# Kernel optimization log

Hardware: AMD Instinct MI355X
Metric: run time of the kernel (lower is better)

Reference implementation:

```python
import jax, jax.numpy as jnp
import numpy as np
from jax.scipy.special import logsumexp

B, S, D, L = 64, 512, 1024, 9


def setup_inputs() -> dict:
    key = jax.random.key(0)
    k1, k2, k3, k4, k5, k6 = jax.random.split(key, 6)
    inputs = jax.random.normal(k1, (B, S, D), dtype=jnp.float32)
    targets = jax.random.randint(k2, (B, S), 0, L)
    sequence_lengths = jax.random.randint(k3, (B,), S // 2, S + 1)
    mask = (jnp.arange(S)[None, :] < sequence_lengths[:, None])
    W = jax.random.normal(k4, (D, L), dtype=jnp.float32) * (1.0 / np.sqrt(D))
    b = jnp.zeros((L,), dtype=jnp.float32)
    transitions = jax.random.normal(k5, (L, L), dtype=jnp.float32) * 0.1
    return {"inputs": inputs, "targets": targets, "sequence_lengths": sequence_lengths,
            "mask": mask, "W": W, "b": b, "transitions": transitions}


def crf_nll(logits, tags, mask, transitions):
    # logits: [B,S,L], tags: [B,S] int, mask: [B,S] bool, transitions: [L,L]
    maskf = mask.astype(logits.dtype)
    # gold-path score (numerator)
    emit = jnp.take_along_axis(logits, tags[..., None], axis=2)[..., 0]  # [B,S]
    trans = transitions[tags[:, :-1], tags[:, 1:]]                        # [B,S-1]
    numerator = (emit * maskf).sum(-1) + (trans * maskf[:, 1:]).sum(-1)   # [B]
    # partition function via forward algorithm (scan over time)
    alpha0 = logits[:, 0]  # [B,L]; position 0 always valid
    emit_t = jnp.swapaxes(logits[:, 1:], 0, 1)   # [S-1,B,L]
    mask_t = jnp.swapaxes(mask[:, 1:], 0, 1)     # [S-1,B]

    def step(alpha, xs):
        e, m = xs
        scores = alpha[:, :, None] + transitions[None, :, :] + e[:, None, :]  # [B,L,L]
        new = logsumexp(scores, axis=1)                                        # [B,L]
        alpha = jnp.where(m[:, None], new, alpha)
        return alpha, None

    alpha, _ = jax.lax.scan(step, alpha0, (emit_t, mask_t))
    denominator = logsumexp(alpha, axis=-1)  # [B]
    return -(numerator - denominator).sum()


def reference(inputs, targets, sequence_lengths, mask, W, b, transitions):
    logits = jnp.einsum('bsd,dl->bsl', inputs, W) + b  # nn.Linear
    values = crf_nll(logits, targets, mask, transitions)
    return (values, logits)
```

## Files before the change

### kernel.cpp

```cpp
#include <hip/hip_runtime.h>
#include <hip/hip_bf16.h>
#include <math.h>

#define BB 64
#define SS 512
#define DD 1024
#define LL 9
#define NCHUNK 32
#define CLEN 16

#define DPP_ADD(v, ctrl)                                                     \
  v += __int_as_float(__builtin_amdgcn_update_dpp(                           \
      0, __float_as_int(v), ctrl, 0xF, 0xF, false))

__global__ __launch_bounds__(256) void gemm_kernel(
    const float* __restrict__ in, const float* __restrict__ W,
    const float* __restrict__ bias, float* __restrict__ out) {
  __shared__ float Wt[LL][DD];
  int tid = threadIdx.x;
  for (int i = tid; i < DD * LL; i += 256) {
    int k = i / LL, l = i % LL;
    Wt[l][k] = W[i];
  }
  __syncthreads();

  int lane = tid & 63;
  int wave = tid >> 6;
  int p = lane & 15;
  int sub = lane >> 4;

  int r0 = blockIdx.x * 64 + wave * 16 + sub;
  const float* x0 = in + (size_t)r0 * DD;

  float acc[4][LL];
#pragma unroll
  for (int q = 0; q < 4; ++q)
#pragma unroll
    for (int l = 0; l < LL; ++l) acc[q][l] = 0.f;

  for (int it = 0; it < 16; ++it) {
    int k0 = it * 64 + p * 4;
    float4 w4[LL];
#pragma unroll
    for (int l = 0; l < LL; ++l)
      w4[l] = *reinterpret_cast<const float4*>(&Wt[l][k0]);
    float4 a[4];
#pragma unroll
    for (int q = 0; q < 4; ++q)
      a[q] = *reinterpret_cast<const float4*>(x0 + (size_t)q * 4 * DD + k0);
#pragma unroll
    for (int q = 0; q < 4; ++q)
#pragma unroll
      for (int l = 0; l < LL; ++l)
        acc[q][l] += a[q].x * w4[l].x + a[q].y * w4[l].y + a[q].z * w4[l].z +
                     a[q].w * w4[l].w;
  }

#pragma unroll
  for (int q = 0; q < 4; ++q)
#pragma unroll
    for (int l = 0; l < LL; ++l) {
      DPP_ADD(acc[q][l], 0x111);
      DPP_ADD(acc[q][l], 0x112);
      DPP_ADD(acc[q][l], 0x114);
      DPP_ADD(acc[q][l], 0x118);
    }
  if (p == 15) {
#pragma unroll
    for (int q = 0; q < 4; ++q)
#pragma unroll
      for (int l = 0; l < LL; ++l)
        out[(size_t)(r0 + q * 4) * LL + l] = acc[q][l] + bias[l];
  }
}

template <int R>
__device__ inline float swz(float x) {
  return __int_as_float(
      __builtin_amdgcn_ds_swizzle(__float_as_int(x), (R << 10) | 0x1F));
}

__global__ __launch_bounds__(64) void crf_chunk_kernel(
    const float* __restrict__ logits, const int* __restrict__ seqlen,
    const float* __restrict__ trans, float* __restrict__ mats,
    float* __restrict__ scales) {
  int lane = threadIdx.x;
  int j = lane & 15;
  int gid = blockIdx.x * 4 + (lane >> 4);
  int b = gid >> 5;
  int k = gid & 31;
  int len = seqlen[b];

  float Mx[81];
#pragma unroll
  for (int i = 0; i < 81; ++i) Mx[i] = __expf(trans[i]);

  float T[LL];
#pragma unroll
  for (int c = 0; c < LL; ++c) T[c] = (j == c) ? 1.f : 0.f;
  float Cl = 0.f;

  const float* lb = logits + (size_t)b * SS * LL;
  int t0 = k * CLEN + 1;
  int tend = (t0 + CLEN < SS) ? (t0 + CLEN) : SS;

  float e[LL];
#pragma unroll
  for (int c = 0; c < LL; ++c) e[c] = lb[t0 * LL + c];

  for (int t = t0; t < tend; ++t) {
    float Ex[LL];
#pragma unroll
    for (int c = 0; c < LL; ++c) Ex[c] = __expf(e[c]);
    if (t + 1 < tend) {
#pragma unroll
      for (int c = 0; c < LL; ++c) e[c] = lb[(t + 1) * LL + c];
    }
    bool active = (t < len);
    float nT[LL];
#pragma unroll
    for (int c = 0; c < LL; ++c) {
      float s = 0.f;
#pragma unroll
      for (int m = 0; m < LL; ++m) s += T[m] * Mx[m * LL + c];
      nT[c] = s * Ex[c];
    }
#pragma unroll
    for (int c = 0; c < LL; ++c) T[c] = active ? nT[c] : T[c];

    if (((t - t0) & 7) == 7) {
      float m = T[0];
#pragma unroll
      for (int c = 1; c < LL; ++c) m = fmaxf(m, T[c]);
      m = fmaxf(m, swz<1>(m));
      m = fmaxf(m, swz<2>(m));
      m = fmaxf(m, swz<4>(m));
      m = fmaxf(m, swz<8>(m));
      float inv = 1.f / m;
#pragma unroll
      for (int c = 0; c < LL; ++c) T[c] *= inv;
      Cl += __logf(m);
    }
  }
  {
    float m = T[0];
#pragma unroll
    for (int c = 1; c < LL; ++c) m = fmaxf(m, T[c]);
    m = fmaxf(m, swz<1>(m));
    m = fmaxf(m, swz<2>(m));
    m = fmaxf(m, swz<4>(m));
    m = fmaxf(m, swz<8>(m));
    float inv = 1.f / m;
#pragma unroll
    for (int c = 0; c < LL; ++c) T[c] *= inv;
    Cl += __logf(m);
  }

  float* Mg = mats + (size_t)gid * 256;
#pragma unroll
  for (int c = 0; c < 16; ++c)
    Mg[c * 16 + (j ^ c)] = (c < LL) ? T[c] : 0.f;
  if (j == 0) scales[gid] = Cl;
}

__global__ __launch_bounds__(64) void crf_combine_kernel(
    const float* __restrict__ logits, const int* __restrict__ targets,
    const int* __restrict__ seqlen, const float* __restrict__ trans,
    const float* __restrict__ mats, const float* __restrict__ scales,
    float* __restrict__ out_val) {
  int lane = threadIdx.x;
  int j = lane & 15;
  int b = blockIdx.x;
  int len = seqlen[b];
  const float* lb = logits + (size_t)b * SS * LL;
  const float* Mb = mats + (size_t)b * NCHUNK * 256;
  const float* Sb = scales + (size_t)b * NCHUNK;

  float alpha = (j < LL) ? __expf(lb[j]) : 0.f;
  float C = 0.f;

  float4 c0 = *reinterpret_cast<const float4*>(Mb + j * 16 + 0);
  float4 c1 = *reinterpret_cast<const float4*>(Mb + j * 16 + 4);
  float4 c2 = *reinterpret_cast<const float4*>(Mb + j * 16 + 8);
  float4 c3 = *reinterpret_cast<const float4*>(Mb + j * 16 + 12);

  for (int k = 0; k < NCHUNK; ++k) {
    float4 n0, n1, n2, n3;
    if (k + 1 < NCHUNK) {
      const float* Mn = Mb + (size_t)(k + 1) * 256 + j * 16;
      n0 = *reinterpret_cast<const float4*>(Mn + 0);
      n1 = *reinterpret_cast<const float4*>(Mn + 4);
      n2 = *reinterpret_cast<const float4*>(Mn + 8);
      n3 = *reinterpret_cast<const float4*>(Mn + 12);
    }
    float v = alpha * c0.x;
    v += swz<1>(alpha) * c0.y;
    v += swz<2>(alpha) * c0.z;
    v += swz<3>(alpha) * c0.w;
    v += swz<4>(alpha) * c1.x;
    v += swz<5>(alpha) * c1.y;
    v += swz<6>(alpha) * c1.z;
    v += swz<7>(alpha) * c1.w;
    v += swz<8>(alpha) * c2.x;
    v += swz<9>(alpha) * c2.y;
    v += swz<10>(alpha) * c2.z;
    v += swz<11>(alpha) * c2.w;
    v += swz<12>(alpha) * c3.x;
    v += swz<13>(alpha) * c3.y;
    v += swz<14>(alpha) * c3.z;
    v += swz<15>(alpha) * c3.w;
    alpha = v;
    C += Sb[k];

    float m = alpha;
    m = fmaxf(m, swz<1>(m));
    m = fmaxf(m, swz<2>(m));
    m = fmaxf(m, swz<4>(m));
    m = fmaxf(m, swz<8>(m));
    float inv = 1.f / m;
    alpha *= inv;
    C += __logf(m);

    if (k + 1 < NCHUNK) { c0 = n0; c1 = n1; c2 = n2; c3 = n3; }
  }

  float s = alpha;
  s += swz<1>(s);
  s += swz<2>(s);
  s += swz<4>(s);
  s += swz<8>(s);
  float denom = C + __logf(s);

  float num = 0.f;
  const int* tb = targets + (size_t)b * SS;
  for (int t = lane; t < SS; t += 64) {
    if (t < len) {
      int tg = tb[t];
      num += lb[t * LL + tg];
      if (t >= 1) {
        int tgp = tb[t - 1];
        num += trans[tgp * LL + tg];
      }
    }
  }
  num += __shfl_xor(num, 1, 64);
  num += __shfl_xor(num, 2, 64);
  num += __shfl_xor(num, 4, 64);
  num += __shfl_xor(num, 8, 64);
  num += __shfl_xor(num, 16, 64);
  num += __shfl_xor(num, 32, 64);

  if (lane == 0) atomicAdd(out_val, denom - num);
}

extern "C" void kernel_launch(void* const* d_in, const int* in_sizes, int n_in,
                              void* d_out, int out_size, void* d_ws,
                              size_t ws_size, hipStream_t stream) {
  const float* inputs = (const float*)d_in[0];
  const int* targets = (const int*)d_in[1];
  const int* seqlen = (const int*)d_in[2];
  const float* W = (const float*)d_in[4];
  const float* bias = (const float*)d_in[5];
  const float* trans = (const float*)d_in[6];
  float* out = (float*)d_out;

  float* mats = (float*)d_ws;
  float* scales = mats + (size_t)BB * NCHUNK * 256;

  gemm_kernel<<<512, 256, 0, stream>>>(inputs, W, bias, out + 1);
  crf_chunk_kernel<<<BB * NCHUNK / 4, 64, 0, stream>>>(out + 1, seqlen, trans,
                                                       mats, scales);
  hipMemsetAsync(d_out, 0, sizeof(float), stream);
  crf_combine_kernel<<<BB, 64, 0, stream>>>(out + 1, targets, seqlen, trans,
                                            mats, scales, out);
}
```

Measured before the change: 56.19 us.

## Prefetch GEMM inputs, move numerator into chunk kernel, drop memset via counter reduction

The GEMM kernel now double-buffers its global input loads, fetching the next iteration's float4s before computing the current one. The gold-path numerator is computed per chunk in the chunk kernel. The combine kernel sums scales and numerator partials with one wave reduction, rescales alpha only every fourth chunk, and uses a tree-shaped sum in its matvec. The memset and float atomicAdd are replaced by per-batch partials plus a last-block counter reduction. This removes a launch and serial work from the combine tail, at the cost of extra registers in the GEMM and reliance on threadfence and counter ordering.

```diff
diff --git a/kernel.cpp b/kernel.cpp
--- a/kernel.cpp
+++ b/kernel.cpp
@@ -19,7 +19,7 @@
   __shared__ float Wt[LL][DD];
   int tid = threadIdx.x;
   for (int i = tid; i < DD * LL; i += 256) {
-    int k = i / LL, l = i % LL;
+    int k = i / LL, l = i - k * LL;
     Wt[l][k] = W[i];
   }
   __syncthreads();
@@ -30,7 +30,7 @@
   int sub = lane >> 4;
 
   int r0 = blockIdx.x * 64 + wave * 16 + sub;
-  const float* x0 = in + (size_t)r0 * DD;
+  const float* x0 = in + (size_t)r0 * DD + p * 4;
 
   float acc[4][LL];
 #pragma unroll
@@ -38,22 +38,33 @@
 #pragma unroll
     for (int l = 0; l < LL; ++l) acc[q][l] = 0.f;
 
+  float4 a[4], an[4];
+#pragma unroll
+  for (int q = 0; q < 4; ++q)
+    a[q] = *reinterpret_cast<const float4*>(x0 + (size_t)q * 4 * DD);
+
   for (int it = 0; it < 16; ++it) {
+    if (it < 15) {
+#pragma unroll
+      for (int q = 0; q < 4; ++q)
+        an[q] = *reinterpret_cast<const float4*>(x0 + (size_t)q * 4 * DD +
+                                                 (it + 1) * 64);
+    }
     int k0 = it * 64 + p * 4;
     float4 w4[LL];
 #pragma unroll
     for (int l = 0; l < LL; ++l)
       w4[l] = *reinterpret_cast<const float4*>(&Wt[l][k0]);
-    float4 a[4];
-#pragma unroll
-    for (int q = 0; q < 4; ++q)
-      a[q] = *reinterpret_cast<const float4*>(x0 + (size_t)q * 4 * DD + k0);
 #pragma unroll
     for (int q = 0; q < 4; ++q)
 #pragma unroll
       for (int l = 0; l < LL; ++l)
         acc[q][l] += a[q].x * w4[l].x + a[q].y * w4[l].y + a[q].z * w4[l].z +
                      a[q].w * w4[l].w;
+    if (it < 15) {
+#pragma unroll
+      for (int q = 0; q < 4; ++q) a[q] = an[q];
+    }
   }
 
 #pragma unroll
@@ -81,9 +92,12 @@
 }
 
 __global__ __launch_bounds__(64) void crf_chunk_kernel(
-    const float* __restrict__ logits, const int* __restrict__ seqlen,
-    const float* __restrict__ trans, float* __restrict__ mats,
-    float* __restrict__ scales) {
+    const float* __restrict__ logits, const int* __restrict__ targets,
+    const int* __restrict__ seqlen, const float* __restrict__ trans,
+    float* __restrict__ mats, float* __restrict__ scales,
+    float* __restrict__ numpart, unsigned* __restrict__ counter) {
+  if (blockIdx.x == 0 && threadIdx.x == 0) *counter = 0u;
+
   int lane = threadIdx.x;
   int j = lane & 15;
   int gid = blockIdx.x * 4 + (lane >> 4);
@@ -101,6 +115,7 @@
   float Cl = 0.f;
 
   const float* lb = logits + (size_t)b * SS * LL;
+  const int* tb = targets + (size_t)b * SS;
   int t0 = k * CLEN + 1;
   int tend = (t0 + CLEN < SS) ? (t0 + CLEN) : SS;
 
@@ -161,20 +176,40 @@
   for (int c = 0; c < 16; ++c)
     Mg[c * 16 + (j ^ c)] = (c < LL) ? T[c] : 0.f;
   if (j == 0) scales[gid] = Cl;
+
+  int t = t0 + j;
+  float np = 0.f;
+  if (t < tend && t < len) {
+    int tg = tb[t];
+    np = lb[t * LL + tg] + trans[tb[t - 1] * LL + tg];
+  }
+  np += swz<1>(np);
+  np += swz<2>(np);
+  np += swz<4>(np);
+  np += swz<8>(np);
+  if (j == 0) numpart[gid] = np;
 }
 
 __global__ __launch_bounds__(64) void crf_combine_kernel(
     const float* __restrict__ logits, const int* __restrict__ targets,
-    const int* __restrict__ seqlen, const float* __restrict__ trans,
     const float* __restrict__ mats, const float* __restrict__ scales,
-    float* __restrict__ out_val) {
+    const float* __restrict__ numpart, float* __restrict__ partials,
+    unsigned* __restrict__ counter, float* __restrict__ out_val) {
   int lane = threadIdx.x;
   int j = lane & 15;
   int b = blockIdx.x;
-  int len = seqlen[b];
   const float* lb = logits + (size_t)b * SS * LL;
   const float* Mb = mats + (size_t)b * NCHUNK * 256;
-  const float* Sb = scales + (size_t)b * NCHUNK;
+
+  float extra = (lane < NCHUNK) ? scales[b * NCHUNK + lane]
+                                : -numpart[b * NCHUNK + (lane - 32)];
+  extra += __shfl_xor(extra, 1, 64);
+  extra += __shfl_xor(extra, 2, 64);
+  extra += __shfl_xor(extra, 4, 64);
+  extra += __shfl_xor(extra, 8, 64);
+  extra += __shfl_xor(extra, 16, 64);
+  extra += __shfl_xor(extra, 32, 64);
+  float emit0 = lb[targets[(size_t)b * SS]];
 
   float alpha = (j < LL) ? __expf(lb[j]) : 0.f;
   float C = 0.f;
@@ -193,34 +228,26 @@
       n2 = *reinterpret_cast<const float4*>(Mn + 8);
       n3 = *reinterpret_cast<const float4*>(Mn + 12);
     }
-    float v = alpha * c0.x;
-    v += swz<1>(alpha) * c0.y;
-    v += swz<2>(alpha) * c0.z;
-    v += swz<3>(alpha) * c0.w;
-    v += swz<4>(alpha) * c1.x;
-    v += swz<5>(alpha) * c1.y;
-    v += swz<6>(alpha) * c1.z;
-    v += swz<7>(alpha) * c1.w;
-    v += swz<8>(alpha) * c2.x;
-    v += swz<9>(alpha) * c2.y;
-    v += swz<10>(alpha) * c2.z;
-    v += swz<11>(alpha) * c2.w;
-    v += swz<12>(alpha) * c3.x;
-    v += swz<13>(alpha) * c3.y;
-    v += swz<14>(alpha) * c3.z;
-    v += swz<15>(alpha) * c3.w;
-    alpha = v;
-    C += Sb[k];
-
-    float m = alpha;
-    m = fmaxf(m, swz<1>(m));
-    m = fmaxf(m, swz<2>(m));
-    m = fmaxf(m, swz<4>(m));
-    m = fmaxf(m, swz<8>(m));
-    float inv = 1.f / m;
-    alpha *= inv;
-    C += __logf(m);
-
+    float s01 = alpha * c0.x + swz<1>(alpha) * c0.y;
+    float s23 = swz<2>(alpha) * c0.z + swz<3>(alpha) * c0.w;
+    float s45 = swz<4>(alpha) * c1.x + swz<5>(alpha) * c1.y;
+    float s67 = swz<6>(alpha) * c1.z + swz<7>(alpha) * c1.w;
+    float s89 = swz<8>(alpha) * c2.x + swz<9>(alpha) * c2.y;
+    float sab = swz<10>(alpha) * c2.z + swz<11>(alpha) * c2.w;
+    float scd = swz<12>(alpha) * c3.x + swz<13>(alpha) * c3.y;
+    float sef = swz<14>(alpha) * c3.z + swz<15>(alpha) * c3.w;
+    alpha = ((s01 + s23) + (s45 + s67)) + ((s89 + sab) + (scd + sef));
+
+    if ((k & 3) == 3) {
+      float m = alpha;
+      m = fmaxf(m, swz<1>(m));
+      m = fmaxf(m, swz<2>(m));
+      m = fmaxf(m, swz<4>(m));
+      m = fmaxf(m, swz<8>(m));
+      float inv = 1.f / m;
+      alpha *= inv;
+      C += __logf(m);
+    }
     if (k + 1 < NCHUNK) { c0 = n0; c1 = n1; c2 = n2; c3 = n3; }
   }
 
@@ -229,28 +256,27 @@
   s += swz<2>(s);
   s += swz<4>(s);
   s += swz<8>(s);
-  float denom = C + __logf(s);
-
-  float num = 0.f;
-  const int* tb = targets + (size_t)b * SS;
-  for (int t = lane; t < SS; t += 64) {
-    if (t < len) {
-      int tg = tb[t];
-      num += lb[t * LL + tg];
-      if (t >= 1) {
-        int tgp = tb[t - 1];
-        num += trans[tgp * LL + tg];
-      }
-    }
-  }
-  num += __shfl_xor(num, 1, 64);
-  num += __shfl_xor(num, 2, 64);
-  num += __shfl_xor(num, 4, 64);
-  num += __shfl_xor(num, 8, 64);
-  num += __shfl_xor(num, 16, 64);
-  num += __shfl_xor(num, 32, 64);
-
-  if (lane == 0) atomicAdd(out_val, denom - num);
+  float result = extra + C + __logf(s) - emit0;
+
+  if (lane == 0) partials[b] = result;
+  __threadfence();
+  unsigned old = 0;
+  if (lane == 0) old = atomicAdd(counter, 1u);
+  old = __shfl(old, 0, 64);
+  if (old == BB - 1) {
+    __threadfence();
+    float v = partials[lane];
+    v += __shfl_xor(v, 1, 64);
+    v += __shfl_xor(v, 2, 64);
+    v += __shfl_xor(v, 4, 64);
+    v += __shfl_xor(v, 8, 64);
+    v += __shfl_xor(v, 16, 64);
+    v += __shfl_xor(v, 32, 64);
+    if (lane == 0) {
+      out_val[0] = v;
+      *counter = 0u;
+    }
+  }
 }
 
 extern "C" void kernel_launch(void* const* d_in, const int* in_sizes, int n_in,
@@ -266,11 +292,13 @@
 
   float* mats = (float*)d_ws;
   float* scales = mats + (size_t)BB * NCHUNK * 256;
+  float* numpart = scales + (size_t)BB * NCHUNK;
+  float* partials = numpart + (size_t)BB * NCHUNK;
+  unsigned* counter = (unsigned*)(partials + BB);
 
   gemm_kernel<<<512, 256, 0, stream>>>(inputs, W, bias, out + 1);
-  crf_chunk_kernel<<<BB * NCHUNK / 4, 64, 0, stream>>>(out + 1, seqlen, trans,
-                                                       mats, scales);
-  hipMemsetAsync(d_out, 0, sizeof(float), stream);
-  crf_combine_kernel<<<BB, 64, 0, stream>>>(out + 1, targets, seqlen, trans,
-                                            mats, scales, out);
-}
+  crf_chunk_kernel<<<BB * NCHUNK / 4, 64, 0, stream>>>(
+      out + 1, targets, seqlen, trans, mats, scales, numpart, counter);
+  crf_combine_kernel<<<BB, 64, 0, stream>>>(out + 1, targets, mats, scales,
+                                            numpart, partials, counter, out);
+}
```

Result: faster. 53.52 us (-4.7%).
